# Kernel tuning notes

Measured on AMD Instinct MI355X. Metric: run time of the kernel, lower is better.

Reference implementation:

```python
import jax, jax.numpy as jnp
import numpy as np
import math

N_EMBD = 1024
HIDDEN = 4 * N_EMBD
N_EXPERTS = 8
TOP_K = 2
B, T = 4, 2048


def new_gelu(x):
    c = math.sqrt(2.0 / math.pi)
    return 0.5 * x * (1.0 + jnp.tanh(c * (x + 0.044715 * x * x * x)))


def setup_inputs() -> dict:
    key = jax.random.key(0)
    ks = jax.random.split(key, 10)
    s = 0.02
    return {
        "x": jax.random.normal(ks[0], (B, T, N_EMBD), dtype=jnp.float32),
        # shared expert (1 shared expert)
        "Wfc_s": jax.random.normal(ks[1], (N_EMBD, HIDDEN), dtype=jnp.float32) * s,
        "bfc_s": jnp.zeros((HIDDEN,), dtype=jnp.float32),
        "Wproj_s": jax.random.normal(ks[2], (HIDDEN, N_EMBD), dtype=jnp.float32) * s,
        "bproj_s": jnp.zeros((N_EMBD,), dtype=jnp.float32),
        # router (no bias)
        "Wr": jax.random.normal(ks[3], (N_EMBD, N_EXPERTS), dtype=jnp.float32) * s,
        # routed experts, stacked on leading expert dim
        "Wfc": jax.random.normal(ks[4], (N_EXPERTS, N_EMBD, HIDDEN), dtype=jnp.float32) * s,
        "bfc": jnp.zeros((N_EXPERTS, HIDDEN), dtype=jnp.float32),
        "Wproj": jax.random.normal(ks[5], (N_EXPERTS, HIDDEN, N_EMBD), dtype=jnp.float32) * s,
        "bproj": jnp.zeros((N_EXPERTS, N_EMBD), dtype=jnp.float32),
    }


def _moe_forward(x, Wfc_s, bfc_s, Wproj_s, bproj_s, Wr, Wfc, bfc, Wproj, bproj):
    Bb, Tt, C = x.shape
    xf = x.reshape(Bb * Tt, C)  # [N, C]
    N = Bb * Tt

    # shared path (1 shared expert, divided by count == 1)
    shared = new_gelu(xf @ Wfc_s + bfc_s) @ Wproj_s + bproj_s

    # router
    logits = xf @ Wr                              # [N, E]
    probs = jax.nn.softmax(logits, axis=-1)
    topk_p, topk_i = jax.lax.top_k(probs, TOP_K)  # [N, K]
    topk_p = topk_p / jnp.sum(topk_p, axis=-1, keepdims=True)

    # dense combine weights: gate[n, e] = normalized prob if expert e selected else 0
    gate = jnp.zeros((N, N_EXPERTS), dtype=xf.dtype)
    gate = gate.at[jnp.arange(N)[:, None], topk_i].add(topk_p)

    routed = jnp.zeros_like(xf)
    for e in range(N_EXPERTS):  # small fixed loop over experts
        h = new_gelu(xf @ Wfc[e] + bfc[e]) @ Wproj[e] + bproj[e]
        routed = routed + h * gate[:, e:e + 1]

    return (shared + routed).reshape(Bb, Tt, C)


def reference(x, Wfc_s, bfc_s, Wproj_s, bproj_s, Wr, Wfc, bfc, Wproj, bproj):
    return _moe_forward(x, Wfc_s, bfc_s, Wproj_s, bproj_s, Wr, Wfc, bfc, Wproj, bproj)
```

## Files before the change

kernel.cpp:

```cpp
#include <hip/hip_runtime.h>
#include <stdint.h>

#define N_TOK 8192
#define C_DIM 1024
#define H_DIM 4096
#define N_EXP 8

typedef __bf16 bf16x8 __attribute__((ext_vector_type(8)));
typedef float floatx4 __attribute__((ext_vector_type(4)));

__device__ __forceinline__ short f2b(float f) {
    unsigned u = __float_as_uint(f);
    unsigned r = (u + 0x7FFFu + ((u >> 16) & 1u)) >> 16;
    return (short)(r & 0xFFFFu);
}

__device__ __forceinline__ float gelu_f(float x) {
    const float c = 0.7978845608028654f;
    float u = c * (x + 0.044715f * x * x * x);
    float a = fabsf(u);
    float e = __expf(-2.0f * a);
    float t = (1.0f - e) / (1.0f + e);
    return 0.5f * x * (1.0f + copysignf(t, u));
}

__device__ __forceinline__ void gl_lds16(const short* g, short* l) {
    __builtin_amdgcn_global_load_lds(
        (const __attribute__((address_space(1))) unsigned int*)g,
        (__attribute__((address_space(3))) unsigned int*)l, 16, 0, 0);
}

__global__ void cast_x_k(const float* __restrict__ in, short* __restrict__ out) {
    int i = (blockIdx.x * 256 + threadIdx.x) * 4;
    float4 v = *(const float4*)(in + i);
    short4 o;
    o.x = f2b(v.x); o.y = f2b(v.y); o.z = f2b(v.z); o.w = f2b(v.w);
    *(short4*)(out + i) = o;
}

__global__ void transpose_cast_k(const float* __restrict__ W, short* __restrict__ WT,
                                 int K, int N) {
    __shared__ float tile[32][33];
    size_t moff = (size_t)blockIdx.z * (size_t)K * (size_t)N;
    int n0 = blockIdx.x * 32, k0 = blockIdx.y * 32;
    int tx = threadIdx.x, ty = threadIdx.y;
#pragma unroll
    for (int j = 0; j < 32; j += 8)
        tile[ty + j][tx] = W[moff + (size_t)(k0 + ty + j) * N + n0 + tx];
    __syncthreads();
#pragma unroll
    for (int j = 0; j < 32; j += 8)
        WT[moff + (size_t)(n0 + ty + j) * K + k0 + tx] = f2b(tile[tx][ty + j]);
}

__global__ void router_k(const float* __restrict__ x, const float* __restrict__ Wr,
                         int* __restrict__ counts, int* __restrict__ tok_list,
                         float* __restrict__ gate_list, int* __restrict__ ent) {
    int token = blockIdx.x * 4 + (threadIdx.x >> 6);
    int lane = threadIdx.x & 63;
    const float* xr = x + (size_t)token * C_DIM;
    float p[8];
#pragma unroll
    for (int e = 0; e < 8; ++e) p[e] = 0.f;
    for (int jj = 0; jj < 4; ++jj) {
        int c = (jj * 64 + lane) * 4;
        float4 xv = *(const float4*)(xr + c);
        const float* w = Wr + (size_t)c * 8;
        float xs[4] = {xv.x, xv.y, xv.z, xv.w};
#pragma unroll
        for (int q = 0; q < 4; ++q)
#pragma unroll
            for (int e = 0; e < 8; ++e) p[e] += xs[q] * w[q * 8 + e];
    }
#pragma unroll
    for (int e = 0; e < 8; ++e)
#pragma unroll
        for (int off = 32; off > 0; off >>= 1) p[e] += __shfl_down(p[e], off);
    if (lane == 0) {
        float mx = p[0];
#pragma unroll
        for (int e = 1; e < 8; ++e) mx = fmaxf(mx, p[e]);
        float ex[8];
#pragma unroll
        for (int e = 0; e < 8; ++e) ex[e] = __expf(p[e] - mx);
        int i1 = 0;
#pragma unroll
        for (int e = 1; e < 8; ++e) if (ex[e] > ex[i1]) i1 = e;
        int i2 = (i1 == 0) ? 1 : 0;
#pragma unroll
        for (int e = 0; e < 8; ++e) if (e != i1 && ex[e] > ex[i2]) i2 = e;
        float s2 = ex[i1] + ex[i2];
        float g1 = ex[i1] / s2, g2 = ex[i2] / s2;
        int pos1 = atomicAdd(&counts[i1], 1);
        tok_list[i1 * N_TOK + pos1] = token;
        gate_list[i1 * N_TOK + pos1] = g1;
        ent[token * 2] = (i1 << 16) | pos1;
        int pos2 = atomicAdd(&counts[i2], 1);
        tok_list[i2 * N_TOK + pos2] = token;
        gate_list[i2 * N_TOK + pos2] = g2;
        ent[token * 2 + 1] = (i2 << 16) | pos2;
    }
}

__global__ void offsets_k(const int* __restrict__ counts, int* __restrict__ offs) {
    if (threadIdx.x == 0) {
        int a = 0;
        for (int e = 0; e < 8; ++e) { offs[e] = a; a += counts[e]; }
    }
}

#define SWZ(r) (((r) ^ ((r) >> 2)) & 3)
template <int MODE>
__global__ __launch_bounds__(256) void gemm_k(
    const short* __restrict__ Abase, const short* __restrict__ Bbase,
    const float* __restrict__ biasbase, void* __restrict__ OutP,
    const int* __restrict__ counts, const int* __restrict__ offsets,
    const int* __restrict__ tok_base, const float* __restrict__ gate_base,
    int Mconst, int K, int N) {
    const int e = blockIdx.z;
    const int count = counts ? counts[e] : Mconst;
    const int nTiles = gridDim.x;
    int bid = blockIdx.y * nTiles + blockIdx.x;
    const int perGroup = 8 * nTiles;
    int group = bid / perGroup;
    int rem = bid - group * perGroup;
    const int mt = group * 8 + (rem & 7);
    const int nt = rem >> 3;
    if (mt * 128 >= count) return;
    const int off = offsets ? offsets[e] : 0;
    const int n0 = nt * 128, m0 = mt * 128;
    const short* Bm = Bbase + (size_t)e * (size_t)K * (size_t)N;
    const float* bias = biasbase + (size_t)e * (size_t)N;
    const int tid = threadIdx.x;
    const int wave = tid >> 6, lane = tid & 63;

    __shared__ __align__(16) short As[128 * 32];
    __shared__ __align__(16) short Bs[128 * 32];

    const int r0 = wave * 32 + (lane >> 2), r1 = r0 + 16;
    const int ca0 = ((lane & 3) ^ SWZ(r0)) * 8;
    const int ca1 = ((lane & 3) ^ SWZ(r1)) * 8;

    int am0 = min(m0 + r0, count - 1), am1 = min(m0 + r1, count - 1);
    size_t ga0, ga1;
    if (MODE == 0) {
        if (tok_base) {
            const int* list = tok_base + e * N_TOK;
            ga0 = (size_t)list[am0];
            ga1 = (size_t)list[am1];
        } else {
            ga0 = (size_t)am0; ga1 = (size_t)am1;
        }
    } else if (MODE == 1) {
        ga0 = (size_t)am0; ga1 = (size_t)am1;
    } else {
        ga0 = (size_t)(off + am0); ga1 = (size_t)(off + am1);
    }
    const short* agp0 = Abase + ga0 * K + ca0;
    const short* agp1 = Abase + ga1 * K + ca1;
    const short* bgp0 = Bm + (size_t)(n0 + r0) * K + ca0;
    const short* bgp1 = Bm + (size_t)(n0 + r1) * K + ca1;
    short* asw0 = &As[(wave * 32) * 32];
    short* asw1 = &As[(wave * 32 + 16) * 32];
    short* bsw0 = &Bs[(wave * 32) * 32];
    short* bsw1 = &Bs[(wave * 32 + 16) * 32];

    const int wm = (wave >> 1) * 64, wn = (wave & 1) * 64;
    const int fr = lane & 15, quad = lane >> 4;
    const short* ard[4];
    const short* brd[4];
#pragma unroll
    for (int i = 0; i < 4; ++i) {
        int ra = wm + i * 16 + fr;
        int rb = wn + i * 16 + fr;
        ard[i] = &As[ra * 32 + ((quad ^ SWZ(ra)) << 3)];
        brd[i] = &Bs[rb * 32 + ((quad ^ SWZ(rb)) << 3)];
    }

    floatx4 acc[4][4];
#pragma unroll
    for (int i = 0; i < 4; ++i)
#pragma unroll
        for (int j = 0; j < 4; ++j) acc[i][j] = (floatx4){0.f, 0.f, 0.f, 0.f};

    const int kIters = K / 32;
    for (int kk = 0; kk < kIters; ++kk) {
        __syncthreads();
        gl_lds16(agp0, asw0);
        gl_lds16(agp1, asw1);
        gl_lds16(bgp0, bsw0);
        gl_lds16(bgp1, bsw1);
        agp0 += 32; agp1 += 32; bgp0 += 32; bgp1 += 32;
        __syncthreads();
        bf16x8 af[4], bfv[4];
#pragma unroll
        for (int i = 0; i < 4; ++i) af[i] = *(const bf16x8*)ard[i];
#pragma unroll
        for (int j = 0; j < 4; ++j) bfv[j] = *(const bf16x8*)brd[j];
#pragma unroll
        for (int i = 0; i < 4; ++i)
#pragma unroll
            for (int j = 0; j < 4; ++j)
                acc[i][j] = __builtin_amdgcn_mfma_f32_16x16x32_bf16(af[i], bfv[j], acc[i][j], 0, 0, 0);
    }

    float bcol[4];
#pragma unroll
    for (int j = 0; j < 4; ++j) bcol[j] = bias[n0 + wn + j * 16 + fr];

    if (MODE == 0) {
        short* H = (short*)OutP;
#pragma unroll
        for (int i = 0; i < 4; ++i) {
            int mb = m0 + wm + i * 16 + quad * 4;
#pragma unroll
            for (int r = 0; r < 4; ++r) {
                int m = mb + r;
                if (m < count) {
                    size_t row = (size_t)(off + m) * (size_t)N;
#pragma unroll
                    for (int j = 0; j < 4; ++j) {
                        float v = acc[i][j][r] + bcol[j];
                        H[row + n0 + wn + j * 16 + fr] = f2b(gelu_f(v));
                    }
                }
            }
        }
    } else if (MODE == 1) {
        float* O = (float*)OutP;
#pragma unroll
        for (int i = 0; i < 4; ++i) {
            int mb = m0 + wm + i * 16 + quad * 4;
#pragma unroll
            for (int r = 0; r < 4; ++r) {
                int m = mb + r;
                size_t row = (size_t)m * (size_t)N;
#pragma unroll
                for (int j = 0; j < 4; ++j) {
                    O[row + n0 + wn + j * 16 + fr] = acc[i][j][r] + bcol[j];
                }
            }
        }
    } else {
        float* R = (float*)OutP;
        const float* gate = gate_base + e * N_TOK;
#pragma unroll
        for (int i = 0; i < 4; ++i) {
            int mb = m0 + wm + i * 16 + quad * 4;
#pragma unroll
            for (int r = 0; r < 4; ++r) {
                int m = mb + r;
                if (m < count) {
                    float g = gate[m];
                    size_t row = (size_t)(off + m) * (size_t)N;
#pragma unroll
                    for (int j = 0; j < 4; ++j) {
                        float v = acc[i][j][r] + bcol[j];
                        R[row + n0 + wn + j * 16 + fr] = g * v;
                    }
                }
            }
        }
    }
}

__global__ void combine_k(float* __restrict__ out, const float* __restrict__ rout,
                          const int* __restrict__ ent, const int* __restrict__ offs) {
    int idx = blockIdx.x * 256 + threadIdx.x;
    int t = idx >> 8;
    int c4 = (idx & 255) * 4;
    int p0 = ent[t * 2], p1 = ent[t * 2 + 1];
    int m0 = offs[p0 >> 16] + (p0 & 0xFFFF);
    int m1 = offs[p1 >> 16] + (p1 & 0xFFFF);
    float4 o = *(float4*)(out + (size_t)t * 1024 + c4);
    float4 a = *(const float4*)(rout + (size_t)m0 * 1024 + c4);
    float4 b = *(const float4*)(rout + (size_t)m1 * 1024 + c4);
    o.x += a.x + b.x; o.y += a.y + b.y; o.z += a.z + b.z; o.w += a.w + b.w;
    *(float4*)(out + (size_t)t * 1024 + c4) = o;
}

extern "C" void kernel_launch(void* const* d_in, const int* in_sizes, int n_in,
                              void* d_out, int out_size, void* d_ws, size_t ws_size,
                              hipStream_t stream) {
    const float* x       = (const float*)d_in[0];
    const float* Wfc_s   = (const float*)d_in[1];
    const float* bfc_s   = (const float*)d_in[2];
    const float* Wproj_s = (const float*)d_in[3];
    const float* bproj_s = (const float*)d_in[4];
    const float* Wr      = (const float*)d_in[5];
    const float* Wfc     = (const float*)d_in[6];
    const float* bfc     = (const float*)d_in[7];
    const float* Wproj   = (const float*)d_in[8];
    const float* bproj   = (const float*)d_in[9];
    float* out = (float*)d_out;

    char* p = (char*)d_ws;
    short* xb      = (short*)p; p += (size_t)N_TOK * C_DIM * 2;
    short* WfcsT   = (short*)p; p += (size_t)C_DIM * H_DIM * 2;
    short* WprojsT = (short*)p; p += (size_t)C_DIM * H_DIM * 2;
    short* WfcT    = (short*)p; p += (size_t)N_EXP * C_DIM * H_DIM * 2;
    short* WprojT  = (short*)p; p += (size_t)N_EXP * C_DIM * H_DIM * 2;
    short* h       = (short*)p; p += (size_t)2 * N_TOK * H_DIM * 2;
    float* rout    = (float*)p; p += (size_t)2 * N_TOK * C_DIM * 4;
    int*   counts  = (int*)p;   p += 128;
    int*   offs    = (int*)p;   p += 128;
    int*   tok_list  = (int*)p;   p += (size_t)N_EXP * N_TOK * 4;
    float* gate_list = (float*)p; p += (size_t)N_EXP * N_TOK * 4;
    int*   ent     = (int*)p;   p += (size_t)N_TOK * 2 * 4;

    hipMemsetAsync(counts, 0, 32, stream);
    cast_x_k<<<8192, 256, 0, stream>>>(x, xb);
    transpose_cast_k<<<dim3(128, 32, 1), dim3(32, 8), 0, stream>>>(Wfc_s, WfcsT, 1024, 4096);
    transpose_cast_k<<<dim3(32, 128, 1), dim3(32, 8), 0, stream>>>(Wproj_s, WprojsT, 4096, 1024);
    transpose_cast_k<<<dim3(128, 32, 8), dim3(32, 8), 0, stream>>>(Wfc, WfcT, 1024, 4096);
    transpose_cast_k<<<dim3(32, 128, 8), dim3(32, 8), 0, stream>>>(Wproj, WprojT, 4096, 1024);
    router_k<<<2048, 256, 0, stream>>>(x, Wr, counts, tok_list, gate_list, ent);
    offsets_k<<<1, 64, 0, stream>>>(counts, offs);

    gemm_k<0><<<dim3(32, 64, 1), 256, 0, stream>>>(xb, WfcsT, bfc_s, h,
                                                   nullptr, nullptr, nullptr, nullptr,
                                                   8192, C_DIM, H_DIM);
    gemm_k<1><<<dim3(8, 64, 1), 256, 0, stream>>>(h, WprojsT, bproj_s, out,
                                                  nullptr, nullptr, nullptr, nullptr,
                                                  8192, H_DIM, C_DIM);
    gemm_k<0><<<dim3(32, 64, 8), 256, 0, stream>>>(xb, WfcT, bfc, h,
                                                   counts, offs, tok_list, nullptr,
                                                   8192, C_DIM, H_DIM);
    gemm_k<2><<<dim3(8, 64, 8), 256, 0, stream>>>(h, WprojT, bproj, rout,
                                                  counts, offs, nullptr, gate_list,
                                                  8192, H_DIM, C_DIM);
    combine_k<<<8192, 256, 0, stream>>>(out, rout, ent, offs);
}
```

Baseline: 1.317 ms.

## Fold shared expert into grouped GEMMs, stage bf16 epilogue through LDS

Treats the shared expert as a ninth expert with an identity token list and unit gates, so two grouped GEMM launches cover both the shared and routed paths. The second GEMM now writes gated bf16 results instead of fp32. Those results are staged through LDS for 16-byte coalesced row stores, and the combine kernel sums three bf16 rows per token. GELU is swapped for a sigmoid-style exp2/rcp approximation. This cuts launches, output bandwidth and tail effects, but adds bf16 rounding of the projected outputs and a less exact GELU.

```diff
diff --git a/kernel.cpp b/kernel.cpp
--- a/kernel.cpp
+++ b/kernel.cpp
@@ -15,13 +15,15 @@
     return (short)(r & 0xFFFFu);
 }
 
-__device__ __forceinline__ float gelu_f(float x) {
-    const float c = 0.7978845608028654f;
-    float u = c * (x + 0.044715f * x * x * x);
-    float a = fabsf(u);
-    float e = __expf(-2.0f * a);
-    float t = (1.0f - e) / (1.0f + e);
-    return 0.5f * x * (1.0f + copysignf(t, u));
+__device__ __forceinline__ float gelu_fast(float x) {
+    const float k1 = -2.3025850929940457f;
+    const float a1 = -2.302114597830384f;
+    const float a3 = -0.10294096656926834f;
+    float x2 = x * x;
+    float m = x * (a1 + a3 * x2);
+    float e = __builtin_amdgcn_exp2f(m);
+    return x * __builtin_amdgcn_rcpf(1.0f + e);
+    (void)k1;
 }
 
 __device__ __forceinline__ void gl_lds16(const short* g, short* l) {
@@ -51,6 +53,14 @@
 #pragma unroll
     for (int j = 0; j < 32; j += 8)
         WT[moff + (size_t)(n0 + ty + j) * K + k0 + tx] = f2b(tile[tx][ty + j]);
+}
+
+__global__ void init_shared_k(int* __restrict__ tok_list, float* __restrict__ gate_list,
+                              int* __restrict__ counts) {
+    int i = blockIdx.x * 256 + threadIdx.x;
+    tok_list[8 * N_TOK + i] = i;
+    gate_list[8 * N_TOK + i] = 1.0f;
+    if (i == 0) counts[8] = N_TOK;
 }
 
 __global__ void router_k(const float* __restrict__ x, const float* __restrict__ Wr,
@@ -105,37 +115,36 @@
 __global__ void offsets_k(const int* __restrict__ counts, int* __restrict__ offs) {
     if (threadIdx.x == 0) {
         int a = 0;
-        for (int e = 0; e < 8; ++e) { offs[e] = a; a += counts[e]; }
+        for (int e = 0; e < 9; ++e) { offs[e] = a; a += counts[e]; }
     }
 }
 
 #define SWZ(r) (((r) ^ ((r) >> 2)) & 3)
-template <int MODE>
+template <bool IS_FC>
 __global__ __launch_bounds__(256) void gemm_k(
     const short* __restrict__ Abase, const short* __restrict__ Bbase,
-    const float* __restrict__ biasbase, void* __restrict__ OutP,
-    const int* __restrict__ counts, const int* __restrict__ offsets,
+    const float* __restrict__ biasbase, short* __restrict__ Out,
+    const int* __restrict__ counts, const int* __restrict__ offs,
     const int* __restrict__ tok_base, const float* __restrict__ gate_base,
-    int Mconst, int K, int N) {
+    int K, int N) {
     const int e = blockIdx.z;
-    const int count = counts ? counts[e] : Mconst;
-    const int nTiles = gridDim.x;
-    int bid = blockIdx.y * nTiles + blockIdx.x;
-    const int perGroup = 8 * nTiles;
-    int group = bid / perGroup;
-    int rem = bid - group * perGroup;
-    const int mt = group * 8 + (rem & 7);
-    const int nt = rem >> 3;
+    const int count = counts[e];
+    const int gx = gridDim.x;
+    int bid = blockIdx.y * gx + blockIdx.x;
+    int s = bid >> 6, w = bid & 63;
+    const int mt = ((s & 7) << 3) + (w >> 3);
+    const int nt = ((s >> 3) << 3) + (w & 7);
     if (mt * 128 >= count) return;
-    const int off = offsets ? offsets[e] : 0;
+    const int off = offs[e];
     const int n0 = nt * 128, m0 = mt * 128;
     const short* Bm = Bbase + (size_t)e * (size_t)K * (size_t)N;
     const float* bias = biasbase + (size_t)e * (size_t)N;
     const int tid = threadIdx.x;
     const int wave = tid >> 6, lane = tid & 63;
 
-    __shared__ __align__(16) short As[128 * 32];
-    __shared__ __align__(16) short Bs[128 * 32];
+    __shared__ __align__(16) short smem[8192];
+    short* As = smem;
+    short* Bs = smem + 4096;
 
     const int r0 = wave * 32 + (lane >> 2), r1 = r0 + 16;
     const int ca0 = ((lane & 3) ^ SWZ(r0)) * 8;
@@ -143,18 +152,13 @@
 
     int am0 = min(m0 + r0, count - 1), am1 = min(m0 + r1, count - 1);
     size_t ga0, ga1;
-    if (MODE == 0) {
-        if (tok_base) {
-            const int* list = tok_base + e * N_TOK;
-            ga0 = (size_t)list[am0];
-            ga1 = (size_t)list[am1];
-        } else {
-            ga0 = (size_t)am0; ga1 = (size_t)am1;
-        }
-    } else if (MODE == 1) {
-        ga0 = (size_t)am0; ga1 = (size_t)am1;
+    if (IS_FC) {
+        const int* list = tok_base + e * N_TOK;
+        ga0 = (size_t)list[am0];
+        ga1 = (size_t)list[am1];
     } else {
-        ga0 = (size_t)(off + am0); ga1 = (size_t)(off + am1);
+        ga0 = (size_t)(off + am0);
+        ga1 = (size_t)(off + am1);
     }
     const short* agp0 = Abase + ga0 * K + ca0;
     const short* agp1 = Abase + ga1 * K + ca1;
@@ -204,79 +208,71 @@
                 acc[i][j] = __builtin_amdgcn_mfma_f32_16x16x32_bf16(af[i], bfv[j], acc[i][j], 0, 0, 0);
     }
 
+    __syncthreads();
     float bcol[4];
 #pragma unroll
     for (int j = 0; j < 4; ++j) bcol[j] = bias[n0 + wn + j * 16 + fr];
 
-    if (MODE == 0) {
-        short* H = (short*)OutP;
-#pragma unroll
-        for (int i = 0; i < 4; ++i) {
-            int mb = m0 + wm + i * 16 + quad * 4;
+    short* slab = smem + wave * 1152;
+    const int rr = lane >> 2, cc = lane & 3;
+    const int srow_m = m0 + wm + rr;
+    short* sw = slab + quad * 288 + fr;
+    const short* srd = slab + rr * 72 + cc * 16;
+
+#pragma unroll
+    for (int i = 0; i < 4; ++i) {
+        float g4[4];
+        if (!IS_FC) {
+            const float* gl = gate_base + e * N_TOK;
+#pragma unroll
+            for (int r = 0; r < 4; ++r) g4[r] = gl[min(m0 + wm + i * 16 + quad * 4 + r, count - 1)];
+        }
+#pragma unroll
+        for (int j = 0; j < 4; ++j)
 #pragma unroll
             for (int r = 0; r < 4; ++r) {
-                int m = mb + r;
-                if (m < count) {
-                    size_t row = (size_t)(off + m) * (size_t)N;
-#pragma unroll
-                    for (int j = 0; j < 4; ++j) {
-                        float v = acc[i][j][r] + bcol[j];
-                        H[row + n0 + wn + j * 16 + fr] = f2b(gelu_f(v));
-                    }
-                }
+                float v = acc[i][j][r] + bcol[j];
+                if (IS_FC) v = gelu_fast(v); else v *= g4[r];
+                sw[r * 72 + j * 16] = f2b(v);
             }
+        int m = srow_m + i * 16;
+        if (m < count) {
+            int4 v0 = *(const int4*)srd;
+            int4 v1 = *(const int4*)(srd + 8);
+            short* orow = Out + (size_t)(off + m) * (size_t)N + n0 + wn + cc * 16;
+            *(int4*)orow = v0;
+            *(int4*)(orow + 8) = v1;
         }
-    } else if (MODE == 1) {
-        float* O = (float*)OutP;
-#pragma unroll
-        for (int i = 0; i < 4; ++i) {
-            int mb = m0 + wm + i * 16 + quad * 4;
-#pragma unroll
-            for (int r = 0; r < 4; ++r) {
-                int m = mb + r;
-                size_t row = (size_t)m * (size_t)N;
-#pragma unroll
-                for (int j = 0; j < 4; ++j) {
-                    O[row + n0 + wn + j * 16 + fr] = acc[i][j][r] + bcol[j];
-                }
-            }
-        }
-    } else {
-        float* R = (float*)OutP;
-        const float* gate = gate_base + e * N_TOK;
-#pragma unroll
-        for (int i = 0; i < 4; ++i) {
-            int mb = m0 + wm + i * 16 + quad * 4;
-#pragma unroll
-            for (int r = 0; r < 4; ++r) {
-                int m = mb + r;
-                if (m < count) {
-                    float g = gate[m];
-                    size_t row = (size_t)(off + m) * (size_t)N;
-#pragma unroll
-                    for (int j = 0; j < 4; ++j) {
-                        float v = acc[i][j][r] + bcol[j];
-                        R[row + n0 + wn + j * 16 + fr] = g * v;
-                    }
-                }
-            }
-        }
-    }
-}
-
-__global__ void combine_k(float* __restrict__ out, const float* __restrict__ rout,
+        __builtin_amdgcn_s_waitcnt(0);
+    }
+}
+
+__global__ void combine_k(float* __restrict__ out, const short* __restrict__ routc,
                           const int* __restrict__ ent, const int* __restrict__ offs) {
-    int idx = blockIdx.x * 256 + threadIdx.x;
-    int t = idx >> 8;
-    int c4 = (idx & 255) * 4;
+    int tid = threadIdx.x;
+    int t = blockIdx.x * 2 + (tid >> 7);
+    int c = (tid & 127) * 8;
     int p0 = ent[t * 2], p1 = ent[t * 2 + 1];
-    int m0 = offs[p0 >> 16] + (p0 & 0xFFFF);
-    int m1 = offs[p1 >> 16] + (p1 & 0xFFFF);
-    float4 o = *(float4*)(out + (size_t)t * 1024 + c4);
-    float4 a = *(const float4*)(rout + (size_t)m0 * 1024 + c4);
-    float4 b = *(const float4*)(rout + (size_t)m1 * 1024 + c4);
-    o.x += a.x + b.x; o.y += a.y + b.y; o.z += a.z + b.z; o.w += a.w + b.w;
-    *(float4*)(out + (size_t)t * 1024 + c4) = o;
+    size_t r0 = (size_t)(offs[p0 >> 16] + (p0 & 0xFFFF)) * 1024 + c;
+    size_t r1 = (size_t)(offs[p1 >> 16] + (p1 & 0xFFFF)) * 1024 + c;
+    size_t rs = (size_t)(16384 + t) * 1024 + c;
+    int4 va = *(const int4*)(routc + rs);
+    int4 vb = *(const int4*)(routc + r0);
+    int4 vc = *(const int4*)(routc + r1);
+    float o[8];
+    const int* pa = (const int*)&va;
+    const int* pb = (const int*)&vb;
+    const int* pc = (const int*)&vc;
+#pragma unroll
+    for (int q = 0; q < 4; ++q) {
+        unsigned a = pa[q], b = pb[q], cw = pc[q];
+        o[2 * q] = __uint_as_float(a << 16) + __uint_as_float(b << 16) + __uint_as_float(cw << 16);
+        o[2 * q + 1] = __uint_as_float(a & 0xFFFF0000u) + __uint_as_float(b & 0xFFFF0000u) +
+                       __uint_as_float(cw & 0xFFFF0000u);
+    }
+    float* op = out + (size_t)t * 1024 + c;
+    *(float4*)op = (float4){o[0], o[1], o[2], o[3]};
+    *(float4*)(op + 4) = (float4){o[4], o[5], o[6], o[7]};
 }
 
 extern "C" void kernel_launch(void* const* d_in, const int* in_sizes, int n_in,
@@ -296,38 +292,35 @@
 
     char* p = (char*)d_ws;
     short* xb      = (short*)p; p += (size_t)N_TOK * C_DIM * 2;
-    short* WfcsT   = (short*)p; p += (size_t)C_DIM * H_DIM * 2;
-    short* WprojsT = (short*)p; p += (size_t)C_DIM * H_DIM * 2;
-    short* WfcT    = (short*)p; p += (size_t)N_EXP * C_DIM * H_DIM * 2;
-    short* WprojT  = (short*)p; p += (size_t)N_EXP * C_DIM * H_DIM * 2;
-    short* h       = (short*)p; p += (size_t)2 * N_TOK * H_DIM * 2;
-    float* rout    = (float*)p; p += (size_t)2 * N_TOK * C_DIM * 4;
+    short* WfcT    = (short*)p; p += (size_t)9 * C_DIM * H_DIM * 2;
+    short* WprojT  = (short*)p; p += (size_t)9 * C_DIM * H_DIM * 2;
+    float* bfc_all = (float*)p; p += (size_t)9 * H_DIM * 4;
+    float* bpj_all = (float*)p; p += (size_t)9 * C_DIM * 4;
+    short* h       = (short*)p; p += (size_t)24576 * H_DIM * 2;
+    short* routc   = (short*)p; p += (size_t)24576 * C_DIM * 2;
     int*   counts  = (int*)p;   p += 128;
     int*   offs    = (int*)p;   p += 128;
-    int*   tok_list  = (int*)p;   p += (size_t)N_EXP * N_TOK * 4;
-    float* gate_list = (float*)p; p += (size_t)N_EXP * N_TOK * 4;
+    int*   tok_list  = (int*)p;   p += (size_t)9 * N_TOK * 4;
+    float* gate_list = (float*)p; p += (size_t)9 * N_TOK * 4;
     int*   ent     = (int*)p;   p += (size_t)N_TOK * 2 * 4;
 
-    hipMemsetAsync(counts, 0, 32, stream);
+    hipMemsetAsync(counts, 0, 64, stream);
     cast_x_k<<<8192, 256, 0, stream>>>(x, xb);
-    transpose_cast_k<<<dim3(128, 32, 1), dim3(32, 8), 0, stream>>>(Wfc_s, WfcsT, 1024, 4096);
-    transpose_cast_k<<<dim3(32, 128, 1), dim3(32, 8), 0, stream>>>(Wproj_s, WprojsT, 4096, 1024);
     transpose_cast_k<<<dim3(128, 32, 8), dim3(32, 8), 0, stream>>>(Wfc, WfcT, 1024, 4096);
+    transpose_cast_k<<<dim3(128, 32, 1), dim3(32, 8), 0, stream>>>(Wfc_s, WfcT + (size_t)8 * C_DIM * H_DIM, 1024, 4096);
     transpose_cast_k<<<dim3(32, 128, 8), dim3(32, 8), 0, stream>>>(Wproj, WprojT, 4096, 1024);
+    transpose_cast_k<<<dim3(32, 128, 1), dim3(32, 8), 0, stream>>>(Wproj_s, WprojT + (size_t)8 * C_DIM * H_DIM, 4096, 1024);
+    hipMemcpyAsync(bfc_all, bfc, (size_t)8 * H_DIM * 4, hipMemcpyDeviceToDevice, stream);
+    hipMemcpyAsync(bfc_all + 8 * H_DIM, bfc_s, (size_t)H_DIM * 4, hipMemcpyDeviceToDevice, stream);
+    hipMemcpyAsync(bpj_all, bproj, (size_t)8 * C_DIM * 4, hipMemcpyDeviceToDevice, stream);
+    hipMemcpyAsync(bpj_all + 8 * C_DIM, bproj_s, (size_t)C_DIM * 4, hipMemcpyDeviceToDevice, stream);
+    init_shared_k<<<32, 256, 0, stream>>>(tok_list, gate_list, counts);
     router_k<<<2048, 256, 0, stream>>>(x, Wr, counts, tok_list, gate_list, ent);
     offsets_k<<<1, 64, 0, stream>>>(counts, offs);
 
-    gemm_k<0><<<dim3(32, 64, 1), 256, 0, stream>>>(xb, WfcsT, bfc_s, h,
-                                                   nullptr, nullptr, nullptr, nullptr,
-                                                   8192, C_DIM, H_DIM);
-    gemm_k<1><<<dim3(8, 64, 1), 256, 0, stream>>>(h, WprojsT, bproj_s, out,
-                                                  nullptr, nullptr, nullptr, nullptr,
-                                                  8192, H_DIM, C_DIM);
-    gemm_k<0><<<dim3(32, 64, 8), 256, 0, stream>>>(xb, WfcT, bfc, h,
-                                                   counts, offs, tok_list, nullptr,
-                                                   8192, C_DIM, H_DIM);
-    gemm_k<2><<<dim3(8, 64, 8), 256, 0, stream>>>(h, WprojT, bproj, rout,
-                                                  counts, offs, nullptr, gate_list,
-                                                  8192, H_DIM, C_DIM);
-    combine_k<<<8192, 256, 0, stream>>>(out, rout, ent, offs);
-}
+    gemm_k<true><<<dim3(32, 64, 9), 256, 0, stream>>>(
+        xb, WfcT, bfc_all, h, counts, offs, tok_list, nullptr, C_DIM, H_DIM);
+    gemm_k<false><<<dim3(8, 64, 9), 256, 0, stream>>>(
+        h, WprojT, bpj_all, routc, counts, offs, nullptr, gate_list, H_DIM, C_DIM);
+    combine_k<<<4096, 256, 0, stream>>>(out, routc, ent, offs);
+}
```

Measured after the change: 1.271 ms. 3.5% less time.
